# Kernel tuning notes

Measured on AMD Instinct MI355X. Metric: run time of the kernel, lower is better.

Reference implementation:

```python
import jax, jax.numpy as jnp
import numpy as np
from jax import lax

B, T, D_IN, H, K, A = 32, 512, 42, 800, 20, 20  # batch, seq, d_in, hidden, linear_out, alphabet_size

def _lstm_dir(x, wih, whh, b, reverse):
    # x: [T,B,D]; wih: [4H,D]; whh: [4H,H]; b: [4H] (b_ih+b_hh merged; mathematically identical)
    xg = jnp.einsum('tbd,hd->tbh', x, wih) + b
    if reverse:
        xg = xg[::-1]
    nh = whh.shape[1]
    h0 = jnp.zeros((x.shape[1], nh), x.dtype)
    def step(carry, xt):
        h, c = carry
        g = xt + h @ whh.T
        i, f, gg, o = jnp.split(g, 4, axis=-1)  # torch gate order i,f,g,o
        c = jax.nn.sigmoid(f) * c + jax.nn.sigmoid(i) * jnp.tanh(gg)
        h = jax.nn.sigmoid(o) * jnp.tanh(c)
        return (h, c), h
    _, hs = lax.scan(step, (h0, h0), xg)
    return hs[::-1] if reverse else hs

_BOND_LENS = jnp.array([145.801, 152.326, 132.868], jnp.float32)  # N-CA, CA-C, C-N (pm)
_BOND_ANGS = jnp.array([2.124, 1.941, 2.028], jnp.float32)

def _coords(tors):
    # tors: [T,B,3] dihedrals -> NeRF-style recursive backbone placement (3 atoms/residue)
    bsz = tors.shape[1]
    a0 = jnp.broadcast_to(jnp.array([0., 0., 1.], jnp.float32), (bsz, 3))
    b0 = jnp.broadcast_to(jnp.array([0., 1., 1.], jnp.float32), (bsz, 3))
    c0 = jnp.broadcast_to(jnp.array([1., 1., 1.], jnp.float32), (bsz, 3))
    def step(carry, tor):
        a, b, c = carry
        outs = []
        for i in range(3):  # three backbone atoms per residue
            r, t, p = _BOND_LENS[i], _BOND_ANGS[i], tor[:, i]
            d2 = jnp.stack([-r * jnp.cos(t) * jnp.ones_like(p),
                            r * jnp.cos(p) * jnp.sin(t),
                            r * jnp.sin(p) * jnp.sin(t)], axis=1)
            bc = c - b
            bc = bc / jnp.linalg.norm(bc, axis=1, keepdims=True)
            n = jnp.cross(b - a, bc)
            n = n / jnp.linalg.norm(n, axis=1, keepdims=True)
            m = jnp.stack([bc, jnp.cross(n, bc), n], axis=2)  # [B,3,3] local frame
            d = jnp.einsum('bij,bj->bi', m, d2) + c
            outs.append(d)
            a, b, c = b, c, d
        return (a, b, c), jnp.stack(outs)
    _, new = lax.scan(step, (a0, b0, c0), tors)  # [T,3,B,3]
    init3 = jnp.stack([a0, b0, c0])
    return jnp.concatenate([init3, new.reshape(-1, bsz, 3)], axis=0)  # [3+3T,B,3]

def _forward(x, wih_l0_f, whh_l0_f, b_l0_f, wih_l0_b, whh_l0_b, b_l0_b,
             wih_l1_f, whh_l1_f, b_l1_f, wih_l1_b, whh_l1_b, b_l1_b,
             lin_w, lin_b, alphabet):
    xs = jnp.transpose(x, (1, 0, 2))  # torch: x.float().transpose(0,1) -> [T,B,D]
    h1 = jnp.concatenate([_lstm_dir(xs, wih_l0_f, whh_l0_f, b_l0_f, False),
                          _lstm_dir(xs, wih_l0_b, whh_l0_b, b_l0_b, True)], axis=-1)
    h2 = jnp.concatenate([_lstm_dir(h1, wih_l1_f, whh_l1_f, b_l1_f, False),
                          _lstm_dir(h1, wih_l1_b, whh_l1_b, b_l1_b, True)], axis=-1)  # [T,B,2H]
    logits = h2 @ lin_w.T + lin_b  # [T,B,K]
    p = jax.nn.softmax(logits, axis=1)  # faithful to nn.Softmax(dim=1) on 3D input (over batch)
    ang = jnp.arctan2(p @ jnp.sin(alphabet), p @ jnp.cos(alphabet))  # [T,B,3] angular mixture
    return _coords(ang)

def setup_inputs():
    key = jax.random.key(0)
    ks = jax.random.split(key, 16)
    s = 0.05
    return {
        'x': jax.random.normal(ks[0], (B, T, D_IN), jnp.float32),
        'wih_l0_f': jax.random.normal(ks[1], (4 * H, D_IN), jnp.float32) * s,
        'whh_l0_f': jax.random.normal(ks[2], (4 * H, H), jnp.float32) * s,
        'b_l0_f': jax.random.normal(ks[3], (4 * H,), jnp.float32) * s,
        'wih_l0_b': jax.random.normal(ks[4], (4 * H, D_IN), jnp.float32) * s,
        'whh_l0_b': jax.random.normal(ks[5], (4 * H, H), jnp.float32) * s,
        'b_l0_b': jax.random.normal(ks[6], (4 * H,), jnp.float32) * s,
        'wih_l1_f': jax.random.normal(ks[7], (4 * H, 2 * H), jnp.float32) * s,
        'whh_l1_f': jax.random.normal(ks[8], (4 * H, H), jnp.float32) * s,
        'b_l1_f': jax.random.normal(ks[9], (4 * H,), jnp.float32) * s,
        'wih_l1_b': jax.random.normal(ks[10], (4 * H, 2 * H), jnp.float32) * s,
        'whh_l1_b': jax.random.normal(ks[11], (4 * H, H), jnp.float32) * s,
        'b_l1_b': jax.random.normal(ks[12], (4 * H,), jnp.float32) * s,
        'lin_w': jax.random.normal(ks[13], (K, 2 * H), jnp.float32) * s,
        'lin_b': jax.random.normal(ks[14], (K,), jnp.float32) * s,
        'alphabet': jax.random.uniform(ks[15], (A, 3), jnp.float32, -np.pi, np.pi),
    }

def reference(x, wih_l0_f, whh_l0_f, b_l0_f, wih_l0_b, whh_l0_b, b_l0_b,
              wih_l1_f, whh_l1_f, b_l1_f, wih_l1_b, whh_l1_b, b_l1_b,
              lin_w, lin_b, alphabet):
    return _forward(x, wih_l0_f, whh_l0_f, b_l0_f, wih_l0_b, whh_l0_b, b_l0_b,
                    wih_l1_f, whh_l1_f, b_l1_f, wih_l1_b, whh_l1_b, b_l1_b,
                    lin_w, lin_b, alphabet)
```

## Files before the change

kernel.cpp:

```cpp
#include <hip/hip_runtime.h>

typedef unsigned short u16;
typedef _Float16 f16x8 __attribute__((ext_vector_type(8)));
typedef float f32x4 __attribute__((ext_vector_type(4)));

#define T_LEN 512
#define BATCH 32
#define DIN 42
#define XPAD 64
#define HID 800
#define G4 3200
#define KCLS 20
#define NBLK 100
#define WSCAN 32
#define HSTR 1664
#define BOFF 832
#define KPAD 1632

__device__ __forceinline__ u16 f2h(float f){
    union { _Float16 h; u16 u; } v; v.h = (_Float16)f; return v.u;
}
__device__ __forceinline__ float sigm(float x){ return 1.f / (1.f + __expf(-x)); }
__device__ __forceinline__ float tanh_(float x){ return 2.f / (1.f + __expf(-2.f * x)) - 1.f; }

__global__ void k_cvt(const float* __restrict__ s, u16* __restrict__ d, int n){
    for (int i = blockIdx.x * blockDim.x + threadIdx.x; i < n; i += gridDim.x * blockDim.x)
        d[i] = f2h(s[i]);
}
__global__ void k_zero16(u16* __restrict__ d, int n){
    for (int i = blockIdx.x * blockDim.x + threadIdx.x; i < n; i += gridDim.x * blockDim.x)
        d[i] = 0;
}
__global__ void k_xT(const float* __restrict__ x, u16* __restrict__ xT){
    const int n = T_LEN * BATCH * XPAD;
    for (int i = blockIdx.x * blockDim.x + threadIdx.x; i < n; i += gridDim.x * blockDim.x){
        int t = i / (BATCH * XPAD);
        int rem = i % (BATCH * XPAD);
        int b = rem / XPAD, k = rem % XPAD;
        xT[i] = (k < DIN) ? f2h(x[((size_t)b * T_LEN + t) * DIN + k]) : (u16)0;
    }
}
__global__ void k_pack2(const float* __restrict__ whh, const float* __restrict__ wih,
                        int nkk, int kin, u16* __restrict__ P2){
    const int n_use = 50 * 2 * nkk * 2 * 64 * 8;
    for (int i = blockIdx.x * blockDim.x + threadIdx.x; i < n_use; i += gridDim.x * blockDim.x){
        int e = i & 7;
        int lane = (i >> 3) & 63;
        int which = (i >> 9) & 1;
        int r = i >> 10;
        int kk = r % nkk;
        int tn = r / nkk;
        int nh = tn & 1, tile = tn >> 1;
        int lr = lane & 15, kgrp = lane >> 4;
        int col = nh * 32 + which * 16 + lr;
        int gate = col >> 4, j = tile * 16 + (col & 15);
        float v;
        if (kk < 25){
            int k = kk * 32 + kgrp * 8 + e;
            v = whh[(size_t)(gate * 800 + j) * 800 + k];
        } else {
            int xk = (kk - 25) * 32 + kgrp * 8 + e;
            v = (xk < kin) ? wih[(size_t)(gate * 800 + j) * kin + xk] : 0.f;
        }
        P2[i] = f2h(v);
    }
}
__global__ void k_pack_bias(const float* __restrict__ b, float* __restrict__ bpk){
    for (int i = blockIdx.x * blockDim.x + threadIdx.x; i < G4; i += gridDim.x * blockDim.x){
        int g = i & 3, j = i >> 2;
        bpk[i] = b[g * 800 + j];
    }
}

__global__ __launch_bounds__(256) void mfma_gemm(
    const u16* __restrict__ A0, const u16* __restrict__ A1, int lda,
    const void* __restrict__ B0_, const void* __restrict__ B1_, int ldb,
    const float* __restrict__ bias0, const float* __restrict__ bias1,
    void* __restrict__ C0, void* __restrict__ C1, int ldc,
    int M, int N, int K, int outmode, int b_is_f32, int khole)
{
    __shared__ u16 At[128 * 40];
    __shared__ u16 Bt[128 * 40];
    const int z = blockIdx.z;
    const u16* Ag = z ? A1 : A0;
    const void* Bg_ = z ? B1_ : B0_;
    const float* bias = z ? bias1 : bias0;
    void* Cg = z ? C1 : C0;
    const u16*   Bu = (const u16*)Bg_;
    const float* Bf = (const float*)Bg_;
    const int tid = threadIdx.x;
    const int lane = tid & 63, w = tid >> 6;
    const int wr = w >> 1, wc = w & 1;
    const int lr = lane & 15, kb8 = (lane >> 4) * 8;
    const int m0 = blockIdx.y * 128, n0 = blockIdx.x * 128;
    const int sr = tid >> 1, skg = (tid & 1) << 4;
    f32x4 acc[4][4] = {};
    const int KT = (K + 31) >> 5;
    for (int kt = 0; kt < KT; ++kt){
        const int k0 = kt << 5;
        __syncthreads();
        {
            size_t base = (size_t)(m0 + sr) * lda + k0 + skg;
            const f16x8* p = (const f16x8*)(Ag + base);
            *(f16x8*)&At[sr * 40 + skg] = p[0];
            *(f16x8*)&At[sr * 40 + skg + 8] = p[1];
        }
        {
            int rn = n0 + sr;
            const int hole = khole && (k0 == 800);
            const int kb = (khole && k0 >= 832) ? (k0 - 32) : k0;
            if (rn < N && !hole && b_is_f32){
                size_t base = (size_t)rn * ldb + kb + skg;
                const float4* p = (const float4*)(Bf + base);
                float4 q0 = p[0], q1 = p[1], q2 = p[2], q3 = p[3];
                f16x8 v0, v1;
                v0[0] = (_Float16)q0.x; v0[1] = (_Float16)q0.y; v0[2] = (_Float16)q0.z; v0[3] = (_Float16)q0.w;
                v0[4] = (_Float16)q1.x; v0[5] = (_Float16)q1.y; v0[6] = (_Float16)q1.z; v0[7] = (_Float16)q1.w;
                v1[0] = (_Float16)q2.x; v1[1] = (_Float16)q2.y; v1[2] = (_Float16)q2.z; v1[3] = (_Float16)q2.w;
                v1[4] = (_Float16)q3.x; v1[5] = (_Float16)q3.y; v1[6] = (_Float16)q3.z; v1[7] = (_Float16)q3.w;
                *(f16x8*)&Bt[sr * 40 + skg] = v0;
                *(f16x8*)&Bt[sr * 40 + skg + 8] = v1;
            } else if (rn < N && !hole){
                size_t base = (size_t)rn * ldb + kb + skg;
                const f16x8* p = (const f16x8*)(Bu + base);
                *(f16x8*)&Bt[sr * 40 + skg] = p[0];
                *(f16x8*)&Bt[sr * 40 + skg + 8] = p[1];
            } else {
                f16x8 zv = {};
                *(f16x8*)&Bt[sr * 40 + skg] = zv;
                *(f16x8*)&Bt[sr * 40 + skg + 8] = zv;
            }
        }
        __syncthreads();
        f16x8 af[4], bfr[4];
        #pragma unroll
        for (int mi = 0; mi < 4; ++mi)
            af[mi] = *(const f16x8*)&At[(wr * 64 + mi * 16 + lr) * 40 + kb8];
        #pragma unroll
        for (int ni = 0; ni < 4; ++ni)
            bfr[ni] = *(const f16x8*)&Bt[(wc * 64 + ni * 16 + lr) * 40 + kb8];
        #pragma unroll
        for (int mi = 0; mi < 4; ++mi)
            #pragma unroll
            for (int ni = 0; ni < 4; ++ni)
                acc[mi][ni] = __builtin_amdgcn_mfma_f32_16x16x32_f16(af[mi], bfr[ni], acc[mi][ni], 0, 0, 0);
    }
    #pragma unroll
    for (int mi = 0; mi < 4; ++mi){
        #pragma unroll
        for (int ni = 0; ni < 4; ++ni){
            int col = n0 + wc * 64 + ni * 16 + lr;
            if (col >= N) continue;
            float bs = bias ? bias[col] : 0.f;
            int pc = (outmode == 2) ? ((col % 800) * 4 + col / 800) : col;
            #pragma unroll
            for (int r = 0; r < 4; ++r){
                int row = m0 + wr * 64 + mi * 16 + ((lane >> 4) * 4 + r);
                float v = acc[mi][ni][r] + bs;
                if (outmode) ((u16*)Cg)[(size_t)row * ldc + pc] = f2h(v);
                else         ((float*)Cg)[(size_t)row * ldc + pc] = v;
            }
        }
    }
}

__global__ __launch_bounds__(256, 1) void scan_coop(
    int nkk, int W, int s0,
    const u16* __restrict__ xTp,
    const u16* __restrict__ xgF, const u16* __restrict__ xgB,
    const u16* __restrict__ P2f, const u16* __restrict__ P2b,
    const float* __restrict__ bpkF, const float* __restrict__ bpkB,
    const u16* __restrict__ hzero, u16* __restrict__ h,
    float* __restrict__ cF, float* __restrict__ cB,
    int cload, int cstore, unsigned* __restrict__ arrive)
{
    __shared__ u16 wlds[2 * 27 * 2 * 64 * 8];
    __shared__ float gLds[32][65];
    const int tid = threadIdx.x;
    const int dir = blockIdx.x & 1;
    const int tile = blockIdx.x >> 1;
    const u16* P2  = dir ? P2b : P2f;
    const u16* xg  = dir ? xgB : xgF;
    const float* bpk = dir ? bpkB : bpkF;
    float* cst = dir ? cB : cF;

    const int wcnt = 2 * nkk * 2 * 64 * 8;
    {
        const u16* src = P2 + (size_t)tile * wcnt;
        for (int i = tid * 8; i < wcnt; i += 256 * 8)
            *(f16x8*)&wlds[i] = *(const f16x8*)&src[i];
    }
    __syncthreads();

    const int lane = tid & 63, w = tid >> 6;
    const int mi = w >> 1, nh = w & 1;
    const int lr = lane & 15, kb8 = (lane >> 4) * 8;
    const int arow = mi * 16 + lr;
    const int b_ep = tid >> 3;
    const int up   = (tid & 7) * 2;
    const int j    = tile * 16 + up;

    float c0 = 0.f, c1 = 0.f;
    if (cload){
        c0 = cst[tile * 512 + tid * 2];
        c1 = cst[tile * 512 + tid * 2 + 1];
    }
    f32x4 bb0 = {}, bb1 = {};
    if (nkk == 27){
        bb0 = *(const f32x4*)(bpk + j * 4);
        bb1 = *(const f32x4*)(bpk + j * 4 + 4);
    }

    const size_t hstep = (size_t)BATCH * HSTR;

    for (int q = 0; q < W; ++q){
        const int s = s0 + q;
        const int t = dir ? (T_LEN - 1 - s) : s;
        const u16* hprev = (s == 0) ? (hzero + dir * BOFF)
                           : (h + (size_t)(dir ? t + 1 : t - 1) * hstep + dir * BOFF);

        const u16* hp = hprev + (size_t)arow * HSTR + kb8;
        f16x8 areg[25];
        #pragma unroll
        for (int kk = 0; kk < 25; ++kk)
            areg[kk] = *(const f16x8*)(hp + kk * 32);
        f16x8 xa0 = {}, xa1 = {}, xv = {};
        if (nkk == 27){
            const u16* xt = xTp + (size_t)t * (BATCH * XPAD) + arow * XPAD + kb8;
            xa0 = *(const f16x8*)(xt);
            xa1 = *(const f16x8*)(xt + 32);
        } else {
            const int qq = dir ? (W - 1 - q) : q;
            xv = *(const f16x8*)(xg + ((size_t)qq * BATCH + b_ep) * G4 + j * 4);
        }

        f32x4 a0a = {}, a0b = {}, a1a = {}, a1b = {};
        #pragma unroll
        for (int kk = 0; kk < 24; kk += 2){
            f16x8 b0e = *(const f16x8*)&wlds[(size_t)((nh * nkk + kk) * 2 + 0) * 512 + lane * 8];
            f16x8 b1e = *(const f16x8*)&wlds[(size_t)((nh * nkk + kk) * 2 + 1) * 512 + lane * 8];
            f16x8 b0o = *(const f16x8*)&wlds[(size_t)((nh * nkk + kk + 1) * 2 + 0) * 512 + lane * 8];
            f16x8 b1o = *(const f16x8*)&wlds[(size_t)((nh * nkk + kk + 1) * 2 + 1) * 512 + lane * 8];
            a0a = __builtin_amdgcn_mfma_f32_16x16x32_f16(areg[kk],     b0e, a0a, 0, 0, 0);
            a1a = __builtin_amdgcn_mfma_f32_16x16x32_f16(areg[kk],     b1e, a1a, 0, 0, 0);
            a0b = __builtin_amdgcn_mfma_f32_16x16x32_f16(areg[kk + 1], b0o, a0b, 0, 0, 0);
            a1b = __builtin_amdgcn_mfma_f32_16x16x32_f16(areg[kk + 1], b1o, a1b, 0, 0, 0);
        }
        {
            f16x8 b0e = *(const f16x8*)&wlds[(size_t)((nh * nkk + 24) * 2 + 0) * 512 + lane * 8];
            f16x8 b1e = *(const f16x8*)&wlds[(size_t)((nh * nkk + 24) * 2 + 1) * 512 + lane * 8];
            a0a = __builtin_amdgcn_mfma_f32_16x16x32_f16(areg[24], b0e, a0a, 0, 0, 0);
            a1a = __builtin_amdgcn_mfma_f32_16x16x32_f16(areg[24], b1e, a1a, 0, 0, 0);
        }
        if (nkk == 27){
            f16x8 b0e = *(const f16x8*)&wlds[(size_t)((nh * nkk + 25) * 2 + 0) * 512 + lane * 8];
            f16x8 b1e = *(const f16x8*)&wlds[(size_t)((nh * nkk + 25) * 2 + 1) * 512 + lane * 8];
            a0b = __builtin_amdgcn_mfma_f32_16x16x32_f16(xa0, b0e, a0b, 0, 0, 0);
            a1b = __builtin_amdgcn_mfma_f32_16x16x32_f16(xa0, b1e, a1b, 0, 0, 0);
            f16x8 b0o = *(const f16x8*)&wlds[(size_t)((nh * nkk + 26) * 2 + 0) * 512 + lane * 8];
            f16x8 b1o = *(const f16x8*)&wlds[(size_t)((nh * nkk + 26) * 2 + 1) * 512 + lane * 8];
            a0a = __builtin_amdgcn_mfma_f32_16x16x32_f16(xa1, b0o, a0a, 0, 0, 0);
            a1a = __builtin_amdgcn_mfma_f32_16x16x32_f16(xa1, b1o, a1a, 0, 0, 0);
        }
        f32x4 acc0 = a0a + a0b;
        f32x4 acc1 = a1a + a1b;
        #pragma unroll
        for (int r = 0; r < 4; ++r){
            int b = mi * 16 + (lane >> 4) * 4 + r;
            gLds[b][nh * 32 + lr]      = acc0[r];
            gLds[b][nh * 32 + 16 + lr] = acc1[r];
        }
        __syncthreads();

        {
            float gi0, gf0, gg0, go0, gi1, gf1, gg1, go1;
            if (nkk == 27){
                gi0 = gLds[b_ep][up]          + bb0[0];
                gf0 = gLds[b_ep][16 + up]     + bb0[1];
                gg0 = gLds[b_ep][32 + up]     + bb0[2];
                go0 = gLds[b_ep][48 + up]     + bb0[3];
                gi1 = gLds[b_ep][up + 1]      + bb1[0];
                gf1 = gLds[b_ep][16 + up + 1] + bb1[1];
                gg1 = gLds[b_ep][32 + up + 1] + bb1[2];
                go1 = gLds[b_ep][48 + up + 1] + bb1[3];
            } else {
                gi0 = gLds[b_ep][up]          + (float)xv[0];
                gf0 = gLds[b_ep][16 + up]     + (float)xv[1];
                gg0 = gLds[b_ep][32 + up]     + (float)xv[2];
                go0 = gLds[b_ep][48 + up]     + (float)xv[3];
                gi1 = gLds[b_ep][up + 1]      + (float)xv[4];
                gf1 = gLds[b_ep][16 + up + 1] + (float)xv[5];
                gg1 = gLds[b_ep][32 + up + 1] + (float)xv[6];
                go1 = gLds[b_ep][48 + up + 1] + (float)xv[7];
            }
            float cn0 = sigm(gf0) * c0 + sigm(gi0) * tanh_(gg0);
            float cn1 = sigm(gf1) * c1 + sigm(gi1) * tanh_(gg1);
            c0 = cn0; c1 = cn1;
            union { unsigned u; _Float16 hh[2]; } pk;
            pk.hh[0] = (_Float16)(sigm(go0) * tanh_(cn0));
            pk.hh[1] = (_Float16)(sigm(go1) * tanh_(cn1));
            unsigned* dst = (unsigned*)(h + (size_t)t * hstep + dir * BOFF + (size_t)b_ep * HSTR + j);
            __hip_atomic_store(dst, pk.u, __ATOMIC_RELAXED, __HIP_MEMORY_SCOPE_AGENT);
        }

        if (q != W - 1){
            const unsigned tgt = (unsigned)(s + 1);
            __syncthreads();
            if (tid == 0)
                __hip_atomic_store(arrive + (size_t)blockIdx.x * 32, tgt,
                                   __ATOMIC_RELAXED, __HIP_MEMORY_SCOPE_AGENT);
            if (tid < 64){
                const unsigned* slot = arrive + (size_t)(((tid < 50) ? tid : 0) * 2 + dir) * 32;
                while (true){
                    unsigned v = __hip_atomic_load(slot, __ATOMIC_RELAXED, __HIP_MEMORY_SCOPE_AGENT);
                    if (__all((int)(v >= tgt))) break;
                    __builtin_amdgcn_s_sleep(1);
                }
            }
            __syncthreads();
        }
    }
    if (cstore){
        cst[tile * 512 + tid * 2]     = c0;
        cst[tile * 512 + tid * 2 + 1] = c1;
    }
}

__global__ __launch_bounds__(64) void k_smax_ang(
    const float* __restrict__ logits, const float* __restrict__ alphabet,
    float* __restrict__ ang)
{
    int t = blockIdx.x;
    __shared__ float P[32][20];
    __shared__ float sA[20][3], cA[20][3];
    int tid = threadIdx.x;
    for (int idx = tid; idx < 32 * 20; idx += 64){
        int b = idx / 20, k = idx % 20;
        P[b][k] = logits[((size_t)t * 32 + b) * 20 + k];
    }
    for (int idx = tid; idx < 60; idx += 64){
        float al = alphabet[idx];
        sA[idx / 3][idx % 3] = sinf(al);
        cA[idx / 3][idx % 3] = cosf(al);
    }
    __syncthreads();
    if (tid < 20){
        float mx = -1e30f;
        for (int b = 0; b < 32; ++b) mx = fmaxf(mx, P[b][tid]);
        float s = 0.f;
        for (int b = 0; b < 32; ++b){ float e = __expf(P[b][tid] - mx); P[b][tid] = e; s += e; }
        float inv = 1.f / s;
        for (int b = 0; b < 32; ++b) P[b][tid] *= inv;
    }
    __syncthreads();
    if (tid < 32){
        float sx = 0, sy = 0, sz = 0, cx = 0, cy = 0, cz = 0;
        for (int k = 0; k < 20; ++k){
            float p = P[tid][k];
            sx += p * sA[k][0]; sy += p * sA[k][1]; sz += p * sA[k][2];
            cx += p * cA[k][0]; cy += p * cA[k][1]; cz += p * cA[k][2];
        }
        size_t base = ((size_t)t * 32 + tid) * 3;
        ang[base + 0] = atan2f(sx, cx);
        ang[base + 1] = atan2f(sy, cy);
        ang[base + 2] = atan2f(sz, cz);
    }
}

__global__ __launch_bounds__(64) void k_coords(const float* __restrict__ ang, float* __restrict__ out){
    int b = threadIdx.x;
    if (b >= 32) return;
    float ax = 0.f, ay = 0.f, az = 1.f;
    float bx = 0.f, by = 1.f, bz = 1.f;
    float cx = 1.f, cy = 1.f, cz = 1.f;
    out[(0 * 32 + b) * 3 + 0] = ax; out[(0 * 32 + b) * 3 + 1] = ay; out[(0 * 32 + b) * 3 + 2] = az;
    out[(1 * 32 + b) * 3 + 0] = bx; out[(1 * 32 + b) * 3 + 1] = by; out[(1 * 32 + b) * 3 + 2] = bz;
    out[(2 * 32 + b) * 3 + 0] = cx; out[(2 * 32 + b) * 3 + 1] = cy; out[(2 * 32 + b) * 3 + 2] = cz;
    const float rr[3] = {145.801f, 152.326f, 132.868f};
    const float ba[3] = {2.124f, 1.941f, 2.028f};
    float ct[3], st[3];
    #pragma unroll
    for (int i = 0; i < 3; ++i){ ct[i] = cosf(ba[i]); st[i] = sinf(ba[i]); }
    for (int t = 0; t < T_LEN; ++t){
        #pragma unroll
        for (int i = 0; i < 3; ++i){
            float p = ang[((size_t)t * 32 + b) * 3 + i];
            float d2x = -rr[i] * ct[i];
            float d2y = rr[i] * cosf(p) * st[i];
            float d2z = rr[i] * sinf(p) * st[i];
            float bcx = cx - bx, bcy = cy - by, bcz = cz - bz;
            float inb = 1.f / sqrtf(bcx * bcx + bcy * bcy + bcz * bcz);
            bcx *= inb; bcy *= inb; bcz *= inb;
            float ux = bx - ax, uy = by - ay, uz = bz - az;
            float nx = uy * bcz - uz * bcy;
            float ny = uz * bcx - ux * bcz;
            float nz = ux * bcy - uy * bcx;
            float inn = 1.f / sqrtf(nx * nx + ny * ny + nz * nz);
            nx *= inn; ny *= inn; nz *= inn;
            float mx = ny * bcz - nz * bcy;
            float my = nz * bcx - nx * bcz;
            float mz = nx * bcy - ny * bcx;
            float dx = bcx * d2x + mx * d2y + nx * d2z + cx;
            float dy = bcy * d2x + my * d2y + ny * d2z + cy;
            float dz = bcz * d2x + mz * d2y + nz * d2z + cz;
            int row = 3 + t * 3 + i;
            out[((size_t)row * 32 + b) * 3 + 0] = dx;
            out[((size_t)row * 32 + b) * 3 + 1] = dy;
            out[((size_t)row * 32 + b) * 3 + 2] = dz;
            ax = bx; ay = by; az = bz;
            bx = cx; by = cy; bz = cz;
            cx = dx; cy = dy; cz = dz;
        }
    }
}

extern "C" void kernel_launch(void* const* d_in, const int* in_sizes, int n_in,
                              void* d_out, int out_size, void* d_ws, size_t ws_size,
                              hipStream_t stream)
{
    const float* x     = (const float*)d_in[0];
    const float* wih0f = (const float*)d_in[1];
    const float* whh0f = (const float*)d_in[2];
    const float* b0f   = (const float*)d_in[3];
    const float* wih0b = (const float*)d_in[4];
    const float* whh0b = (const float*)d_in[5];
    const float* b0b   = (const float*)d_in[6];
    const float* wih1f = (const float*)d_in[7];
    const float* whh1f = (const float*)d_in[8];
    const float* b1f   = (const float*)d_in[9];
    const float* wih1b = (const float*)d_in[10];
    const float* whh1b = (const float*)d_in[11];
    const float* b1b   = (const float*)d_in[12];
    const float* linw  = (const float*)d_in[13];
    const float* linb  = (const float*)d_in[14];
    const float* alpha = (const float*)d_in[15];
    (void)in_sizes; (void)n_in; (void)out_size; (void)ws_size;

    char* ws = (char*)d_ws;
    size_t off = 0;
    auto alloc = [&](size_t bytes) -> void* {
        off = (off + 255) & ~(size_t)255;
        void* p = ws + off;
        off += bytes;
        return p;
    };
    u16* xT     = (u16*)alloc((size_t)T_LEN * BATCH * XPAD * 2);
    u16* h1     = (u16*)alloc((size_t)T_LEN * BATCH * HSTR * 2);
    u16* h2     = (u16*)alloc((size_t)T_LEN * BATCH * HSTR * 2);
    u16* P2_0   = (u16*)alloc((size_t)2 * 50 * 2 * 27 * 2 * 64 * 8 * 2);
    u16* P2_0f  = P2_0;
    u16* P2_0b  = P2_0 + (size_t)50 * 2 * 27 * 2 * 64 * 8;
    u16* P2_1f  = (u16*)alloc((size_t)50 * 2 * 25 * 2 * 64 * 8 * 2);
    u16* P2_1b  = (u16*)alloc((size_t)50 * 2 * 25 * 2 * 64 * 8 * 2);
    u16* linwB  = (u16*)alloc((size_t)KCLS * 1600 * 2);
    float* bpk0f = (float*)alloc((size_t)G4 * 4);
    float* bpk0b = (float*)alloc((size_t)G4 * 4);
    u16* hzero  = (u16*)alloc((size_t)BATCH * HSTR * 2);
    float* c1f  = (float*)alloc((size_t)50 * 512 * 4);
    float* c1b  = (float*)alloc((size_t)50 * 512 * 4);
    u16* xgBc   = (u16*)alloc((size_t)WSCAN * BATCH * G4 * 2);
    unsigned* arrive = (unsigned*)alloc((size_t)NBLK * 32 * 4);
    u16* xgFc = P2_0;
    float* logitsF = (float*)xgFc;
    float* angF    = (float*)xgBc;

    k_zero16<<<dim3(32), dim3(256), 0, stream>>>(hzero, BATCH * HSTR);
    k_cvt<<<dim3(64), dim3(256), 0, stream>>>(linw, linwB, KCLS * 1600);
    k_xT<<<dim3(512), dim3(256), 0, stream>>>(x, xT);
    k_pack2<<<dim3(1024), dim3(256), 0, stream>>>(whh0f, wih0f, 27, DIN, P2_0f);
    k_pack2<<<dim3(1024), dim3(256), 0, stream>>>(whh0b, wih0b, 27, DIN, P2_0b);
    k_pack2<<<dim3(1024), dim3(256), 0, stream>>>(whh1f, nullptr, 25, 0, P2_1f);
    k_pack2<<<dim3(1024), dim3(256), 0, stream>>>(whh1b, nullptr, 25, 0, P2_1b);
    k_pack_bias<<<dim3(8), dim3(256), 0, stream>>>(b0f, bpk0f);
    k_pack_bias<<<dim3(8), dim3(256), 0, stream>>>(b0b, bpk0b);

    const size_t hstep = (size_t)BATCH * HSTR;

    hipMemsetAsync(arrive, 0, (size_t)NBLK * 32 * 4, stream);
    scan_coop<<<dim3(NBLK), dim3(256), 0, stream>>>(
        27, T_LEN, 0,
        xT, nullptr, nullptr,
        P2_0f, P2_0b, bpk0f, bpk0b,
        hzero, h1, nullptr, nullptr, 0, 0, arrive);

    hipMemsetAsync(arrive, 0, (size_t)NBLK * 32 * 4, stream);
    for (int w = 0; w < T_LEN / WSCAN; ++w){
        const int s0  = w * WSCAN;
        const int t0f = s0;
        const int t0b = T_LEN - (w + 1) * WSCAN;
        mfma_gemm<<<dim3(G4 / 128, WSCAN * BATCH / 128, 2), dim3(256), 0, stream>>>(
            h1 + (size_t)t0f * hstep, h1 + (size_t)t0b * hstep, HSTR,
            wih1f, wih1b, 1600, b1f, b1b,
            xgFc, xgBc, G4, WSCAN * BATCH, G4, KPAD, 2, 1, 1);
        scan_coop<<<dim3(NBLK), dim3(256), 0, stream>>>(
            25, WSCAN, s0,
            nullptr, xgFc, xgBc,
            P2_1f, P2_1b, nullptr, nullptr,
            hzero, h2, c1f, c1b, (w > 0) ? 1 : 0, 1, arrive);
    }

    mfma_gemm<<<dim3(1, T_LEN * BATCH / 128, 1), dim3(256), 0, stream>>>(
        h2, h2, HSTR, linwB, linwB, 1600, linb, linb,
        logitsF, logitsF, KCLS, T_LEN * BATCH, KCLS, KPAD, 0, 0, 1);

    k_smax_ang<<<dim3(T_LEN), dim3(64), 0, stream>>>(logitsF, alpha, angF);
    k_coords<<<dim3(1), dim3(64), 0, stream>>>(angF, (float*)d_out);
}
```

Before: 7.287 ms.

## Overlap next-window layer-1 input GEMM with current recurrent scan in one launch

Layer 1 now runs as a fused kernel per window. The first 100 blocks do the recurrent scan over the current window, and 100 extra blocks compute the input-projection GEMM for the next window into double-buffered xg buffers. The window size drops from 32 to 16 so that the GEMM work per launch fits the extra blocks. This hides the separate GEMM launch and its serialization behind the latency-bound scan. The cost is twice as many scan launches, and GEMM blocks competing for CUs and memory bandwidth with the spin-waiting scan blocks.

```diff
diff --git a/kernel.cpp b/kernel.cpp
--- a/kernel.cpp
+++ b/kernel.cpp
@@ -12,7 +12,7 @@
 #define G4 3200
 #define KCLS 20
 #define NBLK 100
-#define WSCAN 32
+#define WSCAN 16
 #define HSTR 1664
 #define BOFF 832
 #define KPAD 1632
@@ -72,27 +72,20 @@
     }
 }
 
-__global__ __launch_bounds__(256) void mfma_gemm(
-    const u16* __restrict__ A0, const u16* __restrict__ A1, int lda,
-    const void* __restrict__ B0_, const void* __restrict__ B1_, int ldb,
-    const float* __restrict__ bias0, const float* __restrict__ bias1,
-    void* __restrict__ C0, void* __restrict__ C1, int ldc,
-    int M, int N, int K, int outmode, int b_is_f32, int khole)
+__device__ void gemm_tile(
+    u16* At, u16* Bt,
+    const u16* __restrict__ Ag, int lda,
+    const void* __restrict__ Bg_, int ldb,
+    const float* __restrict__ bias,
+    void* __restrict__ Cg, int ldc,
+    int N, int K, int m0, int n0, int outmode, int b_is_f32, int khole)
 {
-    __shared__ u16 At[128 * 40];
-    __shared__ u16 Bt[128 * 40];
-    const int z = blockIdx.z;
-    const u16* Ag = z ? A1 : A0;
-    const void* Bg_ = z ? B1_ : B0_;
-    const float* bias = z ? bias1 : bias0;
-    void* Cg = z ? C1 : C0;
     const u16*   Bu = (const u16*)Bg_;
     const float* Bf = (const float*)Bg_;
     const int tid = threadIdx.x;
     const int lane = tid & 63, w = tid >> 6;
     const int wr = w >> 1, wc = w & 1;
     const int lr = lane & 15, kb8 = (lane >> 4) * 8;
-    const int m0 = blockIdx.y * 128, n0 = blockIdx.x * 128;
     const int sr = tid >> 1, skg = (tid & 1) << 4;
     f32x4 acc[4][4] = {};
     const int KT = (K + 31) >> 5;
@@ -164,25 +157,37 @@
     }
 }
 
+__global__ __launch_bounds__(256) void mfma_gemm(
+    const u16* __restrict__ A0, const u16* __restrict__ A1, int lda,
+    const void* __restrict__ B0_, const void* __restrict__ B1_, int ldb,
+    const float* __restrict__ bias0, const float* __restrict__ bias1,
+    void* __restrict__ C0, void* __restrict__ C1, int ldc,
+    int N, int K, int outmode, int b_is_f32, int khole)
+{
+    __shared__ u16 At[128 * 40];
+    __shared__ u16 Bt[128 * 40];
+    const int z = blockIdx.z;
+    gemm_tile(At, Bt, z ? A1 : A0, lda, z ? B1_ : B0_, ldb, z ? bias1 : bias0,
+              z ? C1 : C0, ldc, N, K, blockIdx.y * 128, blockIdx.x * 128,
+              outmode, b_is_f32, khole);
+}
+
+
 __global__ __launch_bounds__(256, 1) void scan_coop(
-    int nkk, int W, int s0,
     const u16* __restrict__ xTp,
-    const u16* __restrict__ xgF, const u16* __restrict__ xgB,
     const u16* __restrict__ P2f, const u16* __restrict__ P2b,
     const float* __restrict__ bpkF, const float* __restrict__ bpkB,
     const u16* __restrict__ hzero, u16* __restrict__ h,
-    float* __restrict__ cF, float* __restrict__ cB,
-    int cload, int cstore, unsigned* __restrict__ arrive)
+    unsigned* __restrict__ arrive)
 {
+    const int nkk = 27;
     __shared__ u16 wlds[2 * 27 * 2 * 64 * 8];
     __shared__ float gLds[32][65];
     const int tid = threadIdx.x;
     const int dir = blockIdx.x & 1;
     const int tile = blockIdx.x >> 1;
     const u16* P2  = dir ? P2b : P2f;
-    const u16* xg  = dir ? xgB : xgF;
     const float* bpk = dir ? bpkB : bpkF;
-    float* cst = dir ? cB : cF;
 
     const int wcnt = 2 * nkk * 2 * 64 * 8;
     {
@@ -201,39 +206,25 @@
     const int j    = tile * 16 + up;
 
     float c0 = 0.f, c1 = 0.f;
-    if (cload){
-        c0 = cst[tile * 512 + tid * 2];
-        c1 = cst[tile * 512 + tid * 2 + 1];
-    }
-    f32x4 bb0 = {}, bb1 = {};
-    if (nkk == 27){
-        bb0 = *(const f32x4*)(bpk + j * 4);
-        bb1 = *(const f32x4*)(bpk + j * 4 + 4);
-    }
-
+    f32x4 bb0 = *(const f32x4*)(bpk + j * 4);
+    f32x4 bb1 = *(const f32x4*)(bpk + j * 4 + 4);
     const size_t hstep = (size_t)BATCH * HSTR;
 
-    for (int q = 0; q < W; ++q){
-        const int s = s0 + q;
+    for (int s = 0; s < T_LEN; ++s){
         const int t = dir ? (T_LEN - 1 - s) : s;
         const u16* hprev = (s == 0) ? (hzero + dir * BOFF)
                            : (h + (size_t)(dir ? t + 1 : t - 1) * hstep + dir * BOFF);
-
         const u16* hp = hprev + (size_t)arow * HSTR + kb8;
         f16x8 areg[25];
         #pragma unroll
         for (int kk = 0; kk < 25; ++kk)
             areg[kk] = *(const f16x8*)(hp + kk * 32);
-        f16x8 xa0 = {}, xa1 = {}, xv = {};
-        if (nkk == 27){
+        f16x8 xa0, xa1;
+        {
             const u16* xt = xTp + (size_t)t * (BATCH * XPAD) + arow * XPAD + kb8;
             xa0 = *(const f16x8*)(xt);
             xa1 = *(const f16x8*)(xt + 32);
-        } else {
-            const int qq = dir ? (W - 1 - q) : q;
-            xv = *(const f16x8*)(xg + ((size_t)qq * BATCH + b_ep) * G4 + j * 4);
-        }
-
+        }
         f32x4 a0a = {}, a0b = {}, a1a = {}, a1b = {};
         #pragma unroll
         for (int kk = 0; kk < 24; kk += 2){
@@ -252,7 +243,7 @@
             a0a = __builtin_amdgcn_mfma_f32_16x16x32_f16(areg[24], b0e, a0a, 0, 0, 0);
             a1a = __builtin_amdgcn_mfma_f32_16x16x32_f16(areg[24], b1e, a1a, 0, 0, 0);
         }
-        if (nkk == 27){
+        {
             f16x8 b0e = *(const f16x8*)&wlds[(size_t)((nh * nkk + 25) * 2 + 0) * 512 + lane * 8];
             f16x8 b1e = *(const f16x8*)&wlds[(size_t)((nh * nkk + 25) * 2 + 1) * 512 + lane * 8];
             a0b = __builtin_amdgcn_mfma_f32_16x16x32_f16(xa0, b0e, a0b, 0, 0, 0);
@@ -271,28 +262,15 @@
             gLds[b][nh * 32 + 16 + lr] = acc1[r];
         }
         __syncthreads();
-
-        {
-            float gi0, gf0, gg0, go0, gi1, gf1, gg1, go1;
-            if (nkk == 27){
-                gi0 = gLds[b_ep][up]          + bb0[0];
-                gf0 = gLds[b_ep][16 + up]     + bb0[1];
-                gg0 = gLds[b_ep][32 + up]     + bb0[2];
-                go0 = gLds[b_ep][48 + up]     + bb0[3];
-                gi1 = gLds[b_ep][up + 1]      + bb1[0];
-                gf1 = gLds[b_ep][16 + up + 1] + bb1[1];
-                gg1 = gLds[b_ep][32 + up + 1] + bb1[2];
-                go1 = gLds[b_ep][48 + up + 1] + bb1[3];
-            } else {
-                gi0 = gLds[b_ep][up]          + (float)xv[0];
-                gf0 = gLds[b_ep][16 + up]     + (float)xv[1];
-                gg0 = gLds[b_ep][32 + up]     + (float)xv[2];
-                go0 = gLds[b_ep][48 + up]     + (float)xv[3];
-                gi1 = gLds[b_ep][up + 1]      + (float)xv[4];
-                gf1 = gLds[b_ep][16 + up + 1] + (float)xv[5];
-                gg1 = gLds[b_ep][32 + up + 1] + (float)xv[6];
-                go1 = gLds[b_ep][48 + up + 1] + (float)xv[7];
-            }
+        {
+            float gi0 = gLds[b_ep][up]          + bb0[0];
+            float gf0 = gLds[b_ep][16 + up]     + bb0[1];
+            float gg0 = gLds[b_ep][32 + up]     + bb0[2];
+            float go0 = gLds[b_ep][48 + up]     + bb0[3];
+            float gi1 = gLds[b_ep][up + 1]      + bb1[0];
+            float gf1 = gLds[b_ep][16 + up + 1] + bb1[1];
+            float gg1 = gLds[b_ep][32 + up + 1] + bb1[2];
+            float go1 = gLds[b_ep][48 + up + 1] + bb1[3];
             float cn0 = sigm(gf0) * c0 + sigm(gi0) * tanh_(gg0);
             float cn1 = sigm(gf1) * c1 + sigm(gi1) * tanh_(gg1);
             c0 = cn0; c1 = cn1;
@@ -302,8 +280,7 @@
             unsigned* dst = (unsigned*)(h + (size_t)t * hstep + dir * BOFF + (size_t)b_ep * HSTR + j);
             __hip_atomic_store(dst, pk.u, __ATOMIC_RELAXED, __HIP_MEMORY_SCOPE_AGENT);
         }
-
-        if (q != W - 1){
+        if (s != T_LEN - 1){
             const unsigned tgt = (unsigned)(s + 1);
             __syncthreads();
             if (tid == 0)
@@ -320,10 +297,154 @@
             __syncthreads();
         }
     }
-    if (cstore){
-        cst[tile * 512 + tid * 2]     = c0;
-        cst[tile * 512 + tid * 2 + 1] = c1;
-    }
+}
+
+__global__ __launch_bounds__(256, 1) void scan_fused(
+    int s0,
+    const u16* __restrict__ xgF, const u16* __restrict__ xgB,
+    const u16* __restrict__ P2f, const u16* __restrict__ P2b,
+    const u16* __restrict__ hzero, u16* __restrict__ h,
+    float* __restrict__ cF, float* __restrict__ cB,
+    int cload, unsigned* __restrict__ arrive,
+    int have_next,
+    const u16* __restrict__ A0n, const u16* __restrict__ A1n,
+    const float* __restrict__ wih1f, const float* __restrict__ wih1b,
+    const float* __restrict__ b1f, const float* __restrict__ b1b,
+    u16* __restrict__ xgFn, u16* __restrict__ xgBn)
+{
+    const int nkk = 25;
+    __shared__ u16 wlds[2 * 27 * 2 * 64 * 8];
+    __shared__ float gLds[32][65];
+    const int tid = threadIdx.x;
+
+    if (blockIdx.x >= NBLK){
+        if (!have_next) return;
+        u16* At = wlds;
+        u16* Bt = wlds + 128 * 40;
+        const int gid = blockIdx.x - NBLK;
+        const int z   = gid & 1;
+        const int grp = gid >> 1;
+        const int cb  = grp % 25;
+        const int mh  = grp / 25;
+        const u16* Ag = z ? A1n : A0n;
+        const float* Bw = z ? wih1b : wih1f;
+        const float* bs = z ? b1b : b1f;
+        u16* Cg = z ? xgBn : xgFn;
+        #pragma unroll
+        for (int mt = 0; mt < 2; ++mt){
+            int m0 = (mh * 2 + mt) * 128;
+            gemm_tile(At, Bt, Ag, HSTR, Bw, 1600, bs, Cg, G4,
+                      G4, KPAD, m0, cb * 128, 2, 1, 1);
+        }
+        return;
+    }
+
+    const int dir = blockIdx.x & 1;
+    const int tile = blockIdx.x >> 1;
+    const u16* P2  = dir ? P2b : P2f;
+    const u16* xg  = dir ? xgB : xgF;
+    float* cst = dir ? cB : cF;
+
+    const int wcnt = 2 * nkk * 2 * 64 * 8;
+    {
+        const u16* src = P2 + (size_t)tile * wcnt;
+        for (int i = tid * 8; i < wcnt; i += 256 * 8)
+            *(f16x8*)&wlds[i] = *(const f16x8*)&src[i];
+    }
+    __syncthreads();
+
+    const int lane = tid & 63, w = tid >> 6;
+    const int mi = w >> 1, nh = w & 1;
+    const int lr = lane & 15, kb8 = (lane >> 4) * 8;
+    const int arow = mi * 16 + lr;
+    const int b_ep = tid >> 3;
+    const int up   = (tid & 7) * 2;
+    const int j    = tile * 16 + up;
+
+    float c0 = 0.f, c1 = 0.f;
+    if (cload){
+        c0 = cst[tile * 512 + tid * 2];
+        c1 = cst[tile * 512 + tid * 2 + 1];
+    }
+    const size_t hstep = (size_t)BATCH * HSTR;
+
+    for (int q = 0; q < WSCAN; ++q){
+        const int s = s0 + q;
+        const int t = dir ? (T_LEN - 1 - s) : s;
+        const u16* hprev = (s == 0) ? (hzero + dir * BOFF)
+                           : (h + (size_t)(dir ? t + 1 : t - 1) * hstep + dir * BOFF);
+        const u16* hp = hprev + (size_t)arow * HSTR + kb8;
+        f16x8 areg[25];
+        #pragma unroll
+        for (int kk = 0; kk < 25; ++kk)
+            areg[kk] = *(const f16x8*)(hp + kk * 32);
+        const int qq = dir ? (WSCAN - 1 - q) : q;
+        f16x8 xv = *(const f16x8*)(xg + ((size_t)qq * BATCH + b_ep) * G4 + j * 4);
+
+        f32x4 a0a = {}, a0b = {}, a1a = {}, a1b = {};
+        #pragma unroll
+        for (int kk = 0; kk < 24; kk += 2){
+            f16x8 b0e = *(const f16x8*)&wlds[(size_t)((nh * nkk + kk) * 2 + 0) * 512 + lane * 8];
+            f16x8 b1e = *(const f16x8*)&wlds[(size_t)((nh * nkk + kk) * 2 + 1) * 512 + lane * 8];
+            f16x8 b0o = *(const f16x8*)&wlds[(size_t)((nh * nkk + kk + 1) * 2 + 0) * 512 + lane * 8];
+            f16x8 b1o = *(const f16x8*)&wlds[(size_t)((nh * nkk + kk + 1) * 2 + 1) * 512 + lane * 8];
+            a0a = __builtin_amdgcn_mfma_f32_16x16x32_f16(areg[kk],     b0e, a0a, 0, 0, 0);
+            a1a = __builtin_amdgcn_mfma_f32_16x16x32_f16(areg[kk],     b1e, a1a, 0, 0, 0);
+            a0b = __builtin_amdgcn_mfma_f32_16x16x32_f16(areg[kk + 1], b0o, a0b, 0, 0, 0);
+            a1b = __builtin_amdgcn_mfma_f32_16x16x32_f16(areg[kk + 1], b1o, a1b, 0, 0, 0);
+        }
+        {
+            f16x8 b0e = *(const f16x8*)&wlds[(size_t)((nh * nkk + 24) * 2 + 0) * 512 + lane * 8];
+            f16x8 b1e = *(const f16x8*)&wlds[(size_t)((nh * nkk + 24) * 2 + 1) * 512 + lane * 8];
+            a0a = __builtin_amdgcn_mfma_f32_16x16x32_f16(areg[24], b0e, a0a, 0, 0, 0);
+            a1a = __builtin_amdgcn_mfma_f32_16x16x32_f16(areg[24], b1e, a1a, 0, 0, 0);
+        }
+        f32x4 acc0 = a0a + a0b;
+        f32x4 acc1 = a1a + a1b;
+        #pragma unroll
+        for (int r = 0; r < 4; ++r){
+            int b = mi * 16 + (lane >> 4) * 4 + r;
+            gLds[b][nh * 32 + lr]      = acc0[r];
+            gLds[b][nh * 32 + 16 + lr] = acc1[r];
+        }
+        __syncthreads();
+        {
+            float gi0 = gLds[b_ep][up]          + (float)xv[0];
+            float gf0 = gLds[b_ep][16 + up]     + (float)xv[1];
+            float gg0 = gLds[b_ep][32 + up]     + (float)xv[2];
+            float go0 = gLds[b_ep][48 + up]     + (float)xv[3];
+            float gi1 = gLds[b_ep][up + 1]      + (float)xv[4];
+            float gf1 = gLds[b_ep][16 + up + 1] + (float)xv[5];
+            float gg1 = gLds[b_ep][32 + up + 1] + (float)xv[6];
+            float go1 = gLds[b_ep][48 + up + 1] + (float)xv[7];
+            float cn0 = sigm(gf0) * c0 + sigm(gi0) * tanh_(gg0);
+            float cn1 = sigm(gf1) * c1 + sigm(gi1) * tanh_(gg1);
+            c0 = cn0; c1 = cn1;
+            union { unsigned u; _Float16 hh[2]; } pk;
+            pk.hh[0] = (_Float16)(sigm(go0) * tanh_(cn0));
+            pk.hh[1] = (_Float16)(sigm(go1) * tanh_(cn1));
+            unsigned* dst = (unsigned*)(h + (size_t)t * hstep + dir * BOFF + (size_t)b_ep * HSTR + j);
+            __hip_atomic_store(dst, pk.u, __ATOMIC_RELAXED, __HIP_MEMORY_SCOPE_AGENT);
+        }
+        if (q != WSCAN - 1){
+            const unsigned tgt = (unsigned)(s + 1);
+            __syncthreads();
+            if (tid == 0)
+                __hip_atomic_store(arrive + (size_t)blockIdx.x * 32, tgt,
+                                   __ATOMIC_RELAXED, __HIP_MEMORY_SCOPE_AGENT);
+            if (tid < 64){
+                const unsigned* slot = arrive + (size_t)(((tid < 50) ? tid : 0) * 2 + dir) * 32;
+                while (true){
+                    unsigned v = __hip_atomic_load(slot, __ATOMIC_RELAXED, __HIP_MEMORY_SCOPE_AGENT);
+                    if (__all((int)(v >= tgt))) break;
+                    __builtin_amdgcn_s_sleep(1);
+                }
+            }
+            __syncthreads();
+        }
+    }
+    cst[tile * 512 + tid * 2]     = c0;
+    cst[tile * 512 + tid * 2 + 1] = c1;
 }
 
 __global__ __launch_bounds__(64) void k_smax_ang(
@@ -444,6 +565,7 @@
         off += bytes;
         return p;
     };
+    const size_t XGC = (size_t)WSCAN * BATCH * G4;
     u16* xT     = (u16*)alloc((size_t)T_LEN * BATCH * XPAD * 2);
     u16* h1     = (u16*)alloc((size_t)T_LEN * BATCH * HSTR * 2);
     u16* h2     = (u16*)alloc((size_t)T_LEN * BATCH * HSTR * 2);
@@ -458,11 +580,14 @@
     u16* hzero  = (u16*)alloc((size_t)BATCH * HSTR * 2);
     float* c1f  = (float*)alloc((size_t)50 * 512 * 4);
     float* c1b  = (float*)alloc((size_t)50 * 512 * 4);
-    u16* xgBc   = (u16*)alloc((size_t)WSCAN * BATCH * G4 * 2);
+    u16* xgBbuf = (u16*)alloc(2 * XGC * 2);
     unsigned* arrive = (unsigned*)alloc((size_t)NBLK * 32 * 4);
-    u16* xgFc = P2_0;
-    float* logitsF = (float*)xgFc;
-    float* angF    = (float*)xgBc;
+    u16* xgF0 = P2_0;
+    u16* xgF1 = P2_0 + XGC;
+    u16* xgB0 = xgBbuf;
+    u16* xgB1 = xgBbuf + XGC;
+    float* logitsF = (float*)P2_1f;
+    float* angF    = (float*)P2_1b;
 
     k_zero16<<<dim3(32), dim3(256), 0, stream>>>(hzero, BATCH * HSTR);
     k_cvt<<<dim3(64), dim3(256), 0, stream>>>(linw, linwB, KCLS * 1600);
@@ -478,30 +603,35 @@
 
     hipMemsetAsync(arrive, 0, (size_t)NBLK * 32 * 4, stream);
     scan_coop<<<dim3(NBLK), dim3(256), 0, stream>>>(
-        27, T_LEN, 0,
-        xT, nullptr, nullptr,
-        P2_0f, P2_0b, bpk0f, bpk0b,
-        hzero, h1, nullptr, nullptr, 0, 0, arrive);
-
+        xT, P2_0f, P2_0b, bpk0f, bpk0b, hzero, h1, arrive);
+
+    const int NW = T_LEN / WSCAN;
     hipMemsetAsync(arrive, 0, (size_t)NBLK * 32 * 4, stream);
-    for (int w = 0; w < T_LEN / WSCAN; ++w){
-        const int s0  = w * WSCAN;
-        const int t0f = s0;
-        const int t0b = T_LEN - (w + 1) * WSCAN;
-        mfma_gemm<<<dim3(G4 / 128, WSCAN * BATCH / 128, 2), dim3(256), 0, stream>>>(
-            h1 + (size_t)t0f * hstep, h1 + (size_t)t0b * hstep, HSTR,
-            wih1f, wih1b, 1600, b1f, b1b,
-            xgFc, xgBc, G4, WSCAN * BATCH, G4, KPAD, 2, 1, 1);
-        scan_coop<<<dim3(NBLK), dim3(256), 0, stream>>>(
-            25, WSCAN, s0,
-            nullptr, xgFc, xgBc,
-            P2_1f, P2_1b, nullptr, nullptr,
-            hzero, h2, c1f, c1b, (w > 0) ? 1 : 0, 1, arrive);
+    mfma_gemm<<<dim3(G4 / 128, WSCAN * BATCH / 128, 2), dim3(256), 0, stream>>>(
+        h1, h1 + (size_t)(T_LEN - WSCAN) * hstep, HSTR,
+        wih1f, wih1b, 1600, b1f, b1b,
+        xgF0, xgB0, G4, G4, KPAD, 2, 1, 1);
+    for (int w = 0; w < NW; ++w){
+        const int s0 = w * WSCAN;
+        u16* xgFc = (w & 1) ? xgF1 : xgF0;
+        u16* xgBc = (w & 1) ? xgB1 : xgB0;
+        u16* xgFn = (w & 1) ? xgF0 : xgF1;
+        u16* xgBn = (w & 1) ? xgB0 : xgB1;
+        const int have_next = (w + 1 < NW);
+        const int t0f_n = (w + 1) * WSCAN;
+        const int t0b_n = T_LEN - (w + 2) * WSCAN;
+        scan_fused<<<dim3(2 * NBLK), dim3(256), 0, stream>>>(
+            s0, xgFc, xgBc, P2_1f, P2_1b, hzero, h2,
+            c1f, c1b, (w > 0) ? 1 : 0, arrive,
+            have_next,
+            h1 + (size_t)(have_next ? t0f_n : 0) * hstep,
+            h1 + (size_t)(have_next ? t0b_n : 0) * hstep,
+            wih1f, wih1b, b1f, b1b, xgFn, xgBn);
     }
 
     mfma_gemm<<<dim3(1, T_LEN * BATCH / 128, 1), dim3(256), 0, stream>>>(
         h2, h2, HSTR, linwB, linwB, 1600, linb, linb,
-        logitsF, logitsF, KCLS, T_LEN * BATCH, KCLS, KPAD, 0, 0, 1);
+        logitsF, logitsF, KCLS, KCLS, KPAD, 0, 0, 1);
 
     k_smax_ang<<<dim3(T_LEN), dim3(64), 0, stream>>>(logitsF, alpha, angF);
     k_coords<<<dim3(1), dim3(64), 0, stream>>>(angF, (float*)d_out);
```

New measurement: 8.309 ms. +14.0%, slower.

## Prefetch next-step inputs, drop trailing barrier, merge weight pack launches

Applied to the files above, without the earlier changes.

Inside the persistent LSTM scan, the next timestep's input-projection or x slice is now loaded before the inter-block barrier, so that load overlaps the wait. Every wavefront now spins on the arrival flags itself, which removes the second __syncthreads after the spin. The four weight-packing launches are merged into one launch with a z grid dimension, cutting launch overhead. Letting all waves poll adds atomic traffic, and removing the barrier depends on each wave seeing the other blocks' h stores without block-level ordering.

```diff
diff --git a/kernel.cpp b/kernel.cpp
--- a/kernel.cpp
+++ b/kernel.cpp
@@ -40,8 +40,17 @@
         xT[i] = (k < DIN) ? f2h(x[((size_t)b * T_LEN + t) * DIN + k]) : (u16)0;
     }
 }
-__global__ void k_pack2(const float* __restrict__ whh, const float* __restrict__ wih,
-                        int nkk, int kin, u16* __restrict__ P2){
+__global__ void k_pack_all(const float* __restrict__ whh0f, const float* __restrict__ wih0f,
+                           const float* __restrict__ whh0b, const float* __restrict__ wih0b,
+                           const float* __restrict__ whh1f, const float* __restrict__ whh1b,
+                           u16* __restrict__ P2_0f, u16* __restrict__ P2_0b,
+                           u16* __restrict__ P2_1f, u16* __restrict__ P2_1b){
+    const int z = blockIdx.z;
+    const float* whh = (z == 0) ? whh0f : (z == 1) ? whh0b : (z == 2) ? whh1f : whh1b;
+    const float* wih = (z == 0) ? wih0f : (z == 1) ? wih0b : nullptr;
+    u16* P2 = (z == 0) ? P2_0f : (z == 1) ? P2_0b : (z == 2) ? P2_1f : P2_1b;
+    const int nkk = (z < 2) ? 27 : 25;
+    const int kin = (z < 2) ? DIN : 0;
     const int n_use = 50 * 2 * nkk * 2 * 64 * 8;
     for (int i = blockIdx.x * blockDim.x + threadIdx.x; i < n_use; i += gridDim.x * blockDim.x){
         int e = i & 7;
@@ -213,6 +222,19 @@
 
     const size_t hstep = (size_t)BATCH * HSTR;
 
+    f16x8 xa0 = {}, xa1 = {}, xv = {};
+    {
+        const int t0 = dir ? (T_LEN - 1 - s0) : s0;
+        if (nkk == 27){
+            const u16* xt = xTp + (size_t)t0 * (BATCH * XPAD) + arow * XPAD + kb8;
+            xa0 = *(const f16x8*)(xt);
+            xa1 = *(const f16x8*)(xt + 32);
+        } else {
+            const int qq = dir ? (W - 1) : 0;
+            xv = *(const f16x8*)(xg + ((size_t)qq * BATCH + b_ep) * G4 + j * 4);
+        }
+    }
+
     for (int q = 0; q < W; ++q){
         const int s = s0 + q;
         const int t = dir ? (T_LEN - 1 - s) : s;
@@ -224,15 +246,6 @@
         #pragma unroll
         for (int kk = 0; kk < 25; ++kk)
             areg[kk] = *(const f16x8*)(hp + kk * 32);
-        f16x8 xa0 = {}, xa1 = {}, xv = {};
-        if (nkk == 27){
-            const u16* xt = xTp + (size_t)t * (BATCH * XPAD) + arow * XPAD + kb8;
-            xa0 = *(const f16x8*)(xt);
-            xa1 = *(const f16x8*)(xt + 32);
-        } else {
-            const int qq = dir ? (W - 1 - q) : q;
-            xv = *(const f16x8*)(xg + ((size_t)qq * BATCH + b_ep) * G4 + j * 4);
-        }
 
         f32x4 a0a = {}, a0b = {}, a1a = {}, a1b = {};
         #pragma unroll
@@ -304,20 +317,29 @@
         }
 
         if (q != W - 1){
+            const int sn = s + 1;
+            if (nkk == 27){
+                const int tn = dir ? (T_LEN - 1 - sn) : sn;
+                const u16* xt = xTp + (size_t)tn * (BATCH * XPAD) + arow * XPAD + kb8;
+                xa0 = *(const f16x8*)(xt);
+                xa1 = *(const f16x8*)(xt + 32);
+            } else {
+                const int qq = dir ? (W - 1 - (q + 1)) : (q + 1);
+                xv = *(const f16x8*)(xg + ((size_t)qq * BATCH + b_ep) * G4 + j * 4);
+            }
             const unsigned tgt = (unsigned)(s + 1);
             __syncthreads();
             if (tid == 0)
                 __hip_atomic_store(arrive + (size_t)blockIdx.x * 32, tgt,
                                    __ATOMIC_RELAXED, __HIP_MEMORY_SCOPE_AGENT);
-            if (tid < 64){
-                const unsigned* slot = arrive + (size_t)(((tid < 50) ? tid : 0) * 2 + dir) * 32;
+            {
+                const unsigned* slot = arrive + (size_t)(((lane < 50) ? lane : 0) * 2 + dir) * 32;
                 while (true){
                     unsigned v = __hip_atomic_load(slot, __ATOMIC_RELAXED, __HIP_MEMORY_SCOPE_AGENT);
                     if (__all((int)(v >= tgt))) break;
                     __builtin_amdgcn_s_sleep(1);
                 }
             }
-            __syncthreads();
         }
     }
     if (cstore){
@@ -467,10 +489,8 @@
     k_zero16<<<dim3(32), dim3(256), 0, stream>>>(hzero, BATCH * HSTR);
     k_cvt<<<dim3(64), dim3(256), 0, stream>>>(linw, linwB, KCLS * 1600);
     k_xT<<<dim3(512), dim3(256), 0, stream>>>(x, xT);
-    k_pack2<<<dim3(1024), dim3(256), 0, stream>>>(whh0f, wih0f, 27, DIN, P2_0f);
-    k_pack2<<<dim3(1024), dim3(256), 0, stream>>>(whh0b, wih0b, 27, DIN, P2_0b);
-    k_pack2<<<dim3(1024), dim3(256), 0, stream>>>(whh1f, nullptr, 25, 0, P2_1f);
-    k_pack2<<<dim3(1024), dim3(256), 0, stream>>>(whh1b, nullptr, 25, 0, P2_1b);
+    k_pack_all<<<dim3(512, 1, 4), dim3(256), 0, stream>>>(
+        whh0f, wih0f, whh0b, wih0b, whh1f, whh1b, P2_0f, P2_0b, P2_1f, P2_1b);
     k_pack_bias<<<dim3(8), dim3(256), 0, stream>>>(b0f, bpk0f);
     k_pack_bias<<<dim3(8), dim3(256), 0, stream>>>(b0b, bpk0b);
 
```

Result: slower. 7.939 ms (+9.0%).
